# Kernel tuning notes

Measured on AMD Instinct MI355X. Metric: run time of the kernel, lower is better.

Reference implementation:

```python
import jax, jax.numpy as jnp
import numpy as np

LN_EPS = 1e-5

def layer_norm(x, gamma, beta):
    mu = jnp.mean(x, axis=-1, keepdims=True)
    var = jnp.mean(jnp.square(x - mu), axis=-1, keepdims=True)
    return (x - mu) * jax.lax.rsqrt(var + LN_EPS) * gamma + beta

def setup_inputs() -> dict:
    key = jax.random.key(0)
    ks = jax.random.split(key, 10)
    B, C, N = 8, 256, 4096
    s = 1.0 / np.sqrt(C)
    inp = {
        "x": jax.random.normal(ks[0], (B, C, N), dtype=jnp.float32),
        "W_qkv": jax.random.uniform(ks[1], (C, C), jnp.float32, -s, s),            # Linear(dim, dim, bias=False)
        "W_mlp": jax.random.uniform(ks[2], (2 * C, 2 * C), jnp.float32, -0.5 * s, 0.5 * s),
        "b_mlp": jax.random.uniform(ks[3], (2 * C,), jnp.float32, -0.5 * s, 0.5 * s),
        "g1": jnp.ones((4 * C,), jnp.float32),
        "beta1": jnp.zeros((4 * C,), jnp.float32),
        "W_res": jax.random.uniform(ks[4], (C, 4 * C), jnp.float32, -0.25 * s, 0.25 * s),  # Linear(4*dim, dim, bias=False)
        "g2": jnp.ones((C,), jnp.float32),
        "beta2": jnp.zeros((C,), jnp.float32),
    }
    return inp

def reference(x, W_qkv, W_mlp, b_mlp, g1, beta1, W_res, g2, beta2):
    # x: (B, C, N) channels-first -> (B, N, C)
    NITER = 2  # niter_heads
    x = jnp.swapaxes(x, 1, 2)
    x = x @ W_qkv.T                                   # shared_qkv, (B, N, C)
    v = jax.lax.stop_gradient(x)                      # x.clone().detach()
    for _ in range(NITER):
        # first_context = x^T @ v : (B, C, C)
        ctx = jnp.einsum('bnc,bnd->bcd', x, v)
        out = jax.nn.softmax(x, axis=-1) @ ctx        # (B, N, C)
        cat1 = jnp.concatenate([out, v], axis=-1)     # (B, N, 2C)
        mlp = jax.nn.relu(cat1 @ W_mlp.T + b_mlp)     # (B, N, 2C)
        cat2 = jnp.concatenate([cat1, mlp], axis=-1)  # (B, N, 4C)
        # dropout layers are identity in eval mode
        v = layer_norm(cat2, g1, beta1) @ W_res.T + x # residual_mlp + skip
        v = layer_norm(x + v, g2, beta2)
    return jnp.swapaxes(v, 1, 2)                      # back to (B, C, N)
```

## Files before the change

kernel.cpp:

```cpp
#include <hip/hip_runtime.h>
#include <cstdint>
#include <cstddef>


using u16 = unsigned short;
using short8 = __attribute__((ext_vector_type(8))) short;
using bf16x8 = __attribute__((ext_vector_type(8))) __bf16;
using f32x4  = __attribute__((ext_vector_type(4))) float;
using i32x4  = __attribute__((ext_vector_type(4))) int;
using u16x4  = __attribute__((ext_vector_type(4))) u16;
using u16x8  = __attribute__((ext_vector_type(8))) u16;

__device__ __forceinline__ float b2f(u16 u) {
    union { unsigned u32; float f; } c; c.u32 = ((unsigned)u) << 16; return c.f;
}
__device__ __forceinline__ u16 f2b(float f) {
    union { float f; unsigned u; } c; c.f = f;
    unsigned r = c.u + 0x7FFFu + ((c.u >> 16) & 1u);
    return (u16)(r >> 16);
}
__device__ __forceinline__ void cvt(u16 a,  u16& o)   { o = a; }
__device__ __forceinline__ void cvt(float a, u16& o)  { o = f2b(a); }
__device__ __forceinline__ void cvt(float a, float& o){ o = a; }
__device__ __forceinline__ void cvt(u16 a,  float& o) { o = b2f(a); }

__device__ __forceinline__ void glds16(const u16* g, short* l) {
    __builtin_amdgcn_global_load_lds(
        (const __attribute__((address_space(1))) void*)g,
        (__attribute__((address_space(3))) void*)l, 16, 0, 0);
}

template<int MODE, int TRF>
__global__ __launch_bounds__(512)
void gemm_bt(const u16* __restrict__ A, const u16* __restrict__ A2,
             const u16* __restrict__ A3,
             int lda, int lda2, int lda3, int kSplit,
             const u16* __restrict__ B, int ldb, long strA, long strB,
             int statStride, int kChunk, int nKsplit,
             float* __restrict__ outF, u16* __restrict__ outB,
             long sOF, long sOB, int ldo,
             const u16* __restrict__ Xres,
             const float* __restrict__ bias,
             const float2* __restrict__ stats,
             const float* __restrict__ g, const float* __restrict__ be)
{
    __shared__ short lsA[128 * 64];
    __shared__ short lsB[128 * 64];

    const unsigned gx = gridDim.x, gy = gridDim.y;
    const unsigned nwg = gx * gy * gridDim.z;
    unsigned lin = blockIdx.x + gx * (blockIdx.y + gy * blockIdx.z);
    lin = (lin & 7u) * (nwg >> 3) + (lin >> 3);
    const unsigned sbx = lin % gx;
    const unsigned rest = lin / gx;
    const unsigned sby = rest % gy;
    const unsigned sbz = rest / gy;

    const int bz    = (int)sbz;
    const int batch = bz / nKsplit;
    const int ks    = bz - batch * nKsplit;
    const u16* Ab = A + (size_t)batch * strA;
    const u16* Bb = B + (size_t)batch * strB;
    const int colBase = (int)sbx * 128;
    const int rowBase = (int)sby * 128;
    const int k0 = ks * kChunk;
    const int k1 = k0 + kChunk;

    const int t    = threadIdx.x;
    const int sRow = t >> 3;
    const int sKl  = (t & 7) << 3;
    const int sKg  = (((t & 7) ^ (sRow & 7)) << 3);

    const int lane = t & 63;
    const int w    = t >> 6;
    const int wr   = (w >> 1) * 32;
    const int wc   = (w & 1) * 64;
    const int mrow = lane & 15;
    const int q    = lane >> 4;

    short* ldA0 = &lsA[w * 512];
    short* ldA1 = &lsA[4096 + w * 512];
    short* ldB0 = &lsB[w * 512];
    short* ldB1 = &lsB[4096 + w * 512];

    float2 st0 = {0.f, 0.f}, st1 = {0.f, 0.f};
    if (TRF == 1) {
        const int sb = batch * statStride + rowBase;
        const float2 t0 = stats[sb + sRow];
        const float2 t1 = stats[sb + sRow + 64];
        st0 = make_float2(0.f, 1.f / t0.y);
        st1 = make_float2(0.f, 1.f / t1.y);
    }

    auto aPtr = [&](int rloc, int kn) -> const u16* {
        const int arow = rowBase + rloc + sRow;
        if (TRF == 2) {
            if (kn < 256)      return A  + (size_t)arow * lda  + kn + sKg;
            else if (kn < 512) return A2 + (size_t)arow * lda2 + (kn - 256) + sKg;
            else               return A3 + (size_t)arow * lda3 + (kn - 512) + sKg;
        } else if (TRF == 3) {
            if (kn < kSplit)   return Ab + (size_t)arow * lda + kn + sKg;
            return A2 + (size_t)arow * lda2 + (kn - kSplit) + sKg;
        }
        return Ab + (size_t)arow * lda + kn + sKg;
    };
    auto loadX = [&](int rloc, int kn, float2 st) -> i32x4 {
        const int arow = rowBase + rloc + sRow;
        i32x4 raw = *(const i32x4*)(Ab + (size_t)arow * lda + kn + sKg);
        short8 h = __builtin_bit_cast(short8, raw);
        short8 o;
#pragma unroll
        for (int i = 0; i < 8; i++) {
            float v = b2f((u16)h[i]);
            v = __expf(v - st.x) * st.y;
            o[i] = (short)f2b(v);
        }
        return __builtin_bit_cast(i32x4, o);
    };

    const f32x4 fzero = {0.f, 0.f, 0.f, 0.f};
    f32x4 acc[2][4];
#pragma unroll
    for (int i = 0; i < 2; i++)
#pragma unroll
        for (int j = 0; j < 4; j++) acc[i][j] = fzero;

    const u16* pB0 = Bb + (size_t)(colBase + sRow) * ldb + sKg;
    const u16* pB1 = pB0 + (size_t)64 * ldb;
    const u16* pA0 = nullptr; const u16* pA1 = nullptr;
    if (TRF == 0) {
        pA0 = Ab + (size_t)(rowBase + sRow) * lda + sKg;
        pA1 = pA0 + (size_t)64 * lda;
    }

    const int rsw = mrow & 7;
    const int kc0 = (((0 * 4 + q) ^ rsw) << 3);
    const int kc1 = (((1 * 4 + q) ^ rsw) << 3);

    i32x4 a0, a1;
    if (TRF == 1) {
        a0 = loadX(0,  k0, st0);
        a1 = loadX(64, k0, st1);
    }

    for (int kk = k0; kk < k1; kk += 64) {
        if (TRF == 1) {
            *(i32x4*)&lsA[sRow * 64 + sKl]        = a0;
            *(i32x4*)&lsA[(sRow + 64) * 64 + sKl] = a1;
        } else if (TRF == 0) {
            glds16(pA0 + kk, ldA0);
            glds16(pA1 + kk, ldA1);
        } else {
            glds16(aPtr(0,  kk), ldA0);
            glds16(aPtr(64, kk), ldA1);
        }
        glds16(pB0 + kk, ldB0);
        glds16(pB1 + kk, ldB1);
        __syncthreads();
        const int kn = kk + 64;
        if (TRF == 1 && kn < k1) {
            a0 = loadX(0,  kn, st0);
            a1 = loadX(64, kn, st1);
        }
#pragma unroll
        for (int h = 0; h < 2; h++) {
            const int kc = h ? kc1 : kc0;
            bf16x8 af[2], bfr[4];
#pragma unroll
            for (int mi = 0; mi < 2; mi++)
                af[mi] = __builtin_bit_cast(bf16x8,
                    *(const short8*)&lsA[(wr + mi * 16 + mrow) * 64 + kc]);
#pragma unroll
            for (int ni = 0; ni < 4; ni++)
                bfr[ni] = __builtin_bit_cast(bf16x8,
                    *(const short8*)&lsB[(wc + ni * 16 + mrow) * 64 + kc]);
#pragma unroll
            for (int mi = 0; mi < 2; mi++)
#pragma unroll
                for (int ni = 0; ni < 4; ni++)
                    acc[mi][ni] = __builtin_amdgcn_mfma_f32_16x16x32_bf16(
                        af[mi], bfr[ni], acc[mi][ni], 0, 0, 0);
        }
        __syncthreads();
    }

    if (MODE == 5) {
        u16* XT = const_cast<u16*>(Xres);
        float2* sm = const_cast<float2*>(stats);
        float rsum[2][4] = {{0.f,0.f,0.f,0.f},{0.f,0.f,0.f,0.f}};
#pragma unroll
        for (int mi = 0; mi < 2; mi++) {
#pragma unroll
            for (int ni = 0; ni < 4; ni++) {
                const int col  = colBase + wc + ni * 16 + mrow;
                const int row0 = rowBase + wr + mi * 16 + q * 4;
                u16x4 hv;
#pragma unroll
                for (int r = 0; r < 4; r++) {
                    const u16 h = f2b(acc[mi][ni][r]);
                    hv[r] = h;
                    outB[(size_t)(row0 + r) * ldo + col] = h;
                    rsum[mi][r] += __expf(b2f(h));
                }
                *(u16x4*)(XT + (size_t)(row0 >> 12) * 1048576
                             + (size_t)col * 4096 + (row0 & 4095)) = hv;
            }
        }
#pragma unroll
        for (int mi = 0; mi < 2; mi++)
#pragma unroll
            for (int r = 0; r < 4; r++) {
                float s = rsum[mi][r];
                s += __shfl_xor(s, 1); s += __shfl_xor(s, 2);
                s += __shfl_xor(s, 4); s += __shfl_xor(s, 8);
                if (mrow == 0)
                    atomicAdd(&sm[rowBase + wr + mi * 16 + q * 4 + r].y, s);
            }
        return;
    }

#pragma unroll
    for (int mi = 0; mi < 2; mi++) {
#pragma unroll
        for (int ni = 0; ni < 4; ni++) {
            const int col = colBase + wc + ni * 16 + mrow;
#pragma unroll
            for (int r = 0; r < 4; r++) {
                const int row = rowBase + wr + mi * 16 + q * 4 + r;
                float v = acc[mi][ni][r];
                if (MODE == 0) {
                    outB[(size_t)batch * sOB + (size_t)row * ldo + col] = f2b(v);
                } else if (MODE == 1) {
                    outB[((size_t)batch * nKsplit + ks) * sOB
                         + (size_t)row * ldo + col] = f2b(v);
                } else if (MODE == 3) {
                    v += bias[col];
                    v = v > 0.f ? v : 0.f;
                    outB[(size_t)row * ldo + col] = f2b(v);
                } else if (MODE == 4) {
                    const float2 ln = stats[row];
                    v = ln.y * (v - ln.x * g[col]) + be[col]
                        + 2.f * b2f(Xres[(size_t)row * 256 + col]);
                    outB[(size_t)row * ldo + col] = f2b(v);
                }
            }
        }
    }
}

template<typename TIN, typename TOUT>
__global__ __launch_bounds__(256)
void transpose_k(const TIN* __restrict__ in, TOUT* __restrict__ out,
                 int R, int Cc, long sIn, long sOut)
{
    __shared__ TOUT tile[32][33];
    const int b = blockIdx.z;
    const TIN* ib = in + (size_t)b * sIn;
    TOUT* ob = out + (size_t)b * sOut;
    const int c0 = blockIdx.x * 32, r0 = blockIdx.y * 32;
    const int tx = threadIdx.x & 31, ty = threadIdx.x >> 5;
#pragma unroll
    for (int i = 0; i < 32; i += 8)
        cvt(ib[(size_t)(r0 + ty + i) * Cc + c0 + tx], tile[ty + i][tx]);
    __syncthreads();
#pragma unroll
    for (int i = 0; i < 32; i += 8)
        ob[(size_t)(c0 + ty + i) * R + r0 + tx] = tile[tx][ty + i];
}

__global__ __launch_bounds__(256)
void stats1024_k(const u16* __restrict__ OUT, const u16* __restrict__ V,
                 const u16* __restrict__ MLPo, float2* __restrict__ st)
{
    const int wave = threadIdx.x >> 6, lane = threadIdx.x & 63;
    const size_t row = (size_t)blockIdx.x * 4 + wave;
    const int c = lane * 16;
    const u16* src;
    if (c < 256)       src = OUT  + row * 256 + c;
    else if (c < 512)  src = V    + row * 256 + (c - 256);
    else               src = MLPo + row * 512 + (c - 512);
    short8 r0 = *(const short8*)(src);
    short8 r1 = *(const short8*)(src + 8);
    float s = 0.f, s2 = 0.f;
#pragma unroll
    for (int i = 0; i < 8; i++) {
        const float a = b2f((u16)r0[i]), b = b2f((u16)r1[i]);
        s += a + b; s2 += a * a + b * b;
    }
    for (int o = 32; o > 0; o >>= 1) { s += __shfl_xor(s, o); s2 += __shfl_xor(s2, o); }
    const float mean = s * (1.f / 1024.f);
    const float var  = s2 * (1.f / 1024.f) - mean * mean;
    if (lane == 0) st[row] = make_float2(mean, rsqrtf(var + 1e-5f));
}

template<typename OUTT, bool WRITE_VB>
__global__ __launch_bounds__(256)
void ln256t_k(const u16* __restrict__ Tb, const float* __restrict__ g,
              const float* __restrict__ be, u16* __restrict__ Vb,
              OUTT* __restrict__ outT)
{
    constexpr int STRIDE = (sizeof(OUTT) == 2) ? 266 : 261;
    __shared__ OUTT tile[32 * STRIDE];
    const int wid = threadIdx.x >> 6, lane = threadIdx.x & 63;
    const int bx = blockIdx.x;
    const size_t r0 = (size_t)bx * 32;
    const int b  = bx >> 7;
    const int n0 = (bx & 127) * 32;

#pragma unroll
    for (int j = 0; j < 8; j++) {
        const int lr = wid * 8 + j;
        const size_t row = r0 + lr;
        const u16x4 tb = *(const u16x4*)(Tb + row * 256 + lane * 4);
        const float x0 = b2f(tb.x), x1 = b2f(tb.y), x2 = b2f(tb.z), x3 = b2f(tb.w);
        float s  = x0 + x1 + x2 + x3;
        float s2 = x0 * x0 + x1 * x1 + x2 * x2 + x3 * x3;
        for (int o = 32; o > 0; o >>= 1) { s += __shfl_xor(s, o); s2 += __shfl_xor(s2, o); }
        const float mean = s * (1.f / 256.f);
        const float var  = s2 * (1.f / 256.f) - mean * mean;
        const float rstd = rsqrtf(var + 1e-5f);
        const int c = lane * 4;
        float4 ov = { (x0 - mean) * rstd * g[c + 0] + be[c + 0],
                      (x1 - mean) * rstd * g[c + 1] + be[c + 1],
                      (x2 - mean) * rstd * g[c + 2] + be[c + 2],
                      (x3 - mean) * rstd * g[c + 3] + be[c + 3] };
        if (WRITE_VB) {
            u16x4 vb = { f2b(ov.x), f2b(ov.y), f2b(ov.z), f2b(ov.w) };
            *(u16x4*)(Vb + row * 256 + c) = vb;
        }
        OUTT* tl = &tile[lr * STRIDE + c];
        cvt(ov.x, tl[0]); cvt(ov.y, tl[1]); cvt(ov.z, tl[2]); cvt(ov.w, tl[3]);
    }
    __syncthreads();

    const int c = threadIdx.x;
    OUTT* dst = outT + ((size_t)b * 256 + c) * 4096 + n0;
    if (sizeof(OUTT) == 2) {
#pragma unroll
        for (int k = 0; k < 4; k++) {
            u16x8 v;
#pragma unroll
            for (int i = 0; i < 8; i++) v[i] = *(const u16*)&tile[(k * 8 + i) * STRIDE + c];
            *(u16x8*)((u16*)dst + k * 8) = v;
        }
    } else {
#pragma unroll
        for (int k = 0; k < 8; k++) {
            float4 v;
            v.x = *(const float*)&tile[(k * 4 + 0) * STRIDE + c];
            v.y = *(const float*)&tile[(k * 4 + 1) * STRIDE + c];
            v.z = *(const float*)&tile[(k * 4 + 2) * STRIDE + c];
            v.w = *(const float*)&tile[(k * 4 + 3) * STRIDE + c];
            *(float4*)((float*)dst + k * 4) = v;
        }
    }
}

__global__ __launch_bounds__(256)
void ctxreduce_k(const u16* __restrict__ ctxp, u16* __restrict__ ctxb)
{
    const int i = blockIdx.x * 256 + threadIdx.x;
    const int batch  = i >> 14;
    const int within = i & 16383;
    const u16x4* src = (const u16x4*)ctxp + (size_t)batch * 16 * 16384 + within;
    float4 s = {0.f, 0.f, 0.f, 0.f};
#pragma unroll
    for (int ks = 0; ks < 16; ks++) {
        const u16x4 v = src[(size_t)ks * 16384];
        s.x += b2f(v.x); s.y += b2f(v.y); s.z += b2f(v.z); s.w += b2f(v.w);
    }
    u16x4 o = { f2b(s.x), f2b(s.y), f2b(s.z), f2b(s.w) };
    ((u16x4*)ctxb)[i] = o;
}

__global__ __launch_bounds__(256)
void wconv_k(const float* __restrict__ Wq, const float* __restrict__ Wm,
             u16* __restrict__ oq, u16* __restrict__ om)
{
    const int i = blockIdx.x * 256 + threadIdx.x;
    const float* src; u16* dst; int j;
    if (i < 16384) { src = Wq; dst = oq; j = i; }
    else           { src = Wm; dst = om; j = i - 16384; }
    const float4 v = ((const float4*)src)[j];
    u16x4 o = { f2b(v.x), f2b(v.y), f2b(v.z), f2b(v.w) };
    ((u16x4*)dst)[j] = o;
}

__global__ __launch_bounds__(256)
void wresprep_k(const float* __restrict__ Wres, const float* __restrict__ g1,
                const float* __restrict__ be1, u16* __restrict__ Wr_b,
                float* __restrict__ sg, float* __restrict__ br,
                float2* __restrict__ smst)
{
    const int tid = blockIdx.x * 256 + threadIdx.x;
    smst[tid * 2]     = make_float2(0.f, 0.f);
    smst[tid * 2 + 1] = make_float2(0.f, 0.f);

    const int wv = threadIdx.x >> 6, lane = threadIdx.x & 63;
    const int row = blockIdx.x * 4 + wv;
    const float* src = Wres + (size_t)row * 1024;
    float s = 0.f, b = 0.f;
#pragma unroll
    for (int j = 0; j < 4; j++) {
        const int c = j * 256 + lane * 4;
        const float4 w  = *(const float4*)(src + c);
        const float4 gg = *(const float4*)(g1 + c);
        const float4 bb = *(const float4*)(be1 + c);
        const float4 wg = { w.x * gg.x, w.y * gg.y, w.z * gg.z, w.w * gg.w };
        u16x4 o = { f2b(wg.x), f2b(wg.y), f2b(wg.z), f2b(wg.w) };
        *(u16x4*)(Wr_b + (size_t)row * 1024 + c) = o;
        s += wg.x + wg.y + wg.z + wg.w;
        b += w.x * bb.x + w.y * bb.y + w.z * bb.z + w.w * bb.w;
    }
    for (int o = 32; o > 0; o >>= 1) { s += __shfl_xor(s, o); b += __shfl_xor(b, o); }
    if (lane == 0) { sg[row] = s; br[row] = b; }
}

extern "C" void kernel_launch(void* const* d_in, const int* in_sizes, int n_in,
                              void* d_out, int out_size, void* d_ws, size_t ws_size,
                              hipStream_t stream)
{
    (void)in_sizes; (void)n_in; (void)out_size; (void)ws_size;
    const float* x    = (const float*)d_in[0];
    const float* Wqkv = (const float*)d_in[1];
    const float* Wmlp = (const float*)d_in[2];
    const float* bmlp = (const float*)d_in[3];
    const float* g1   = (const float*)d_in[4];
    const float* be1  = (const float*)d_in[5];
    const float* Wres = (const float*)d_in[6];
    const float* g2   = (const float*)d_in[7];
    const float* be2  = (const float*)d_in[8];

    char* ws = (char*)d_ws;
    u16*    Xb   = (u16*)ws;    ws += (size_t)16777216;
    u16*    XT   = (u16*)ws;    ws += (size_t)16777216;
    u16*    Vb   = (u16*)ws;    ws += (size_t)16777216;
    u16*    VT2  = (u16*)ws;    ws += (size_t)16777216;
    u16*    OUT  = (u16*)ws;    ws += (size_t)16777216;
    u16*    MLPo = (u16*)ws;    ws += (size_t)33554432;
    u16*    Tb   = (u16*)ws;    ws += (size_t)16777216;
    u16*    ctxp = (u16*)ws;    ws += (size_t)16777216;
    u16*    ctxb = (u16*)ws;    ws += (size_t)1048576;
    float2* smst = (float2*)ws; ws += (size_t)262144;
    float2* lnst = (float2*)ws; ws += (size_t)262144;
    u16*    Wq_b = (u16*)ws;    ws += (size_t)131072;
    u16*    Wm_b = (u16*)ws;    ws += (size_t)524288;
    u16*    Wr_b = (u16*)ws;    ws += (size_t)524288;
    float*  sg   = (float*)ws;  ws += (size_t)1024;
    float*  br   = (float*)ws;  ws += (size_t)1024;
    u16*    xt   = MLPo;

    wconv_k<<<dim3(320), 256, 0, stream>>>(Wqkv, Wmlp, Wq_b, Wm_b);
    wresprep_k<<<dim3(64), 256, 0, stream>>>(Wres, g1, be1, Wr_b, sg, br, smst);

    transpose_k<float, u16><<<dim3(128, 8, 8), 256, 0, stream>>>(
        x, xt, 256, 4096, 256L * 4096, 4096L * 256);

    gemm_bt<5, 0><<<dim3(2, 256, 1), 512, 0, stream>>>(
        xt, nullptr, nullptr, 256, 0, 0, 0, Wq_b, 256, 0, 0, 0, 256, 1,
        nullptr, Xb, 0, 0, 256, XT, nullptr, smst, nullptr, nullptr);

    const u16* VTcur = XT;
    const u16* Vcur  = Xb;

    for (int it = 0; it < 2; ++it) {
        gemm_bt<1, 0><<<dim3(2, 2, 128), 512, 0, stream>>>(
            VTcur, nullptr, nullptr, 4096, 0, 0, 0, XT, 4096,
            1048576, 1048576, 0, 256, 16,
            nullptr, ctxp, 0, 65536, 256, nullptr, nullptr, nullptr, nullptr, nullptr);
        ctxreduce_k<<<dim3(512), 256, 0, stream>>>(ctxp, ctxb);

        gemm_bt<0, 1><<<dim3(2, 32, 8), 512, 0, stream>>>(
            Xb, nullptr, nullptr, 256, 0, 0, 0, ctxb, 256,
            1048576, 65536, 4096, 256, 1,
            nullptr, OUT, 0, 1048576, 256, nullptr, nullptr, smst, nullptr, nullptr);

        gemm_bt<3, 3><<<dim3(4, 256, 1), 512, 0, stream>>>(
            OUT, Vcur, nullptr, 256, 256, 0, 256, Wm_b, 512, 0, 0, 0, 512, 1,
            nullptr, MLPo, 0, 0, 512, nullptr, bmlp, nullptr, nullptr, nullptr);

        stats1024_k<<<dim3(8192), 256, 0, stream>>>(OUT, Vcur, MLPo, lnst);

        gemm_bt<4, 2><<<dim3(2, 256, 1), 512, 0, stream>>>(
            OUT, Vcur, MLPo, 256, 256, 512, 0, Wr_b, 1024, 0, 0, 0, 1024, 1,
            nullptr, Tb, 0, 0, 256, Xb, nullptr, lnst, sg, br);

        if (it == 0) {
            ln256t_k<u16, true><<<dim3(1024), 256, 0, stream>>>(
                Tb, g2, be2, Vb, VT2);
            VTcur = VT2;
            Vcur  = Vb;
        } else {
            ln256t_k<float, false><<<dim3(1024), 256, 0, stream>>>(
                Tb, g2, be2, nullptr, (float*)d_out);
        }
    }
}
```

Measured before the change: 327.9 us.

## Fuse LayerNorm-1024 row statistics into the residual GEMM's A-tile loads

Removes the separate stats1024 kernel, which re-read OUT, V and MLPo to compute per-row mean and variance. The residual GEMM (MODE 4) now accumulates sum and sum-of-squares from each A tile already staged in shared memory, reduces them across lanes and through a small LDS array, then applies the normalization in the epilogue. This saves one kernel launch and a full 1024-wide activation read per iteration. The cost is extra LDS reads and ALU work inside the GEMM main loop, plus an added barrier in the epilogue.

```diff
diff --git a/kernel.cpp b/kernel.cpp
--- a/kernel.cpp
+++ b/kernel.cpp
@@ -46,6 +46,7 @@
 {
     __shared__ short lsA[128 * 64];
     __shared__ short lsB[128 * 64];
+    __shared__ float2 lstat[128];
 
     const unsigned gx = gridDim.x, gy = gridDim.y;
     const unsigned nwg = gx * gy * gridDim.z;
@@ -136,6 +137,8 @@
     const int rsw = mrow & 7;
     const int kc0 = (((0 * 4 + q) ^ rsw) << 3);
     const int kc1 = (((1 * 4 + q) ^ rsw) << 3);
+
+    float stA = 0.f, stA2 = 0.f, stB = 0.f, stB2 = 0.f;
 
     i32x4 a0, a1;
     if (TRF == 1) {
@@ -162,6 +165,17 @@
             a0 = loadX(0,  kn, st0);
             a1 = loadX(64, kn, st1);
         }
+        if (MODE == 4) {
+            short8 c0 = *(const short8*)&lsA[sRow * 64 + sKl];
+            short8 c1 = *(const short8*)&lsA[(sRow + 64) * 64 + sKl];
+#pragma unroll
+            for (int i = 0; i < 8; i++) {
+                const float v0 = b2f((u16)c0[i]);
+                const float v1 = b2f((u16)c1[i]);
+                stA += v0; stA2 += v0 * v0;
+                stB += v1; stB2 += v1 * v1;
+            }
+        }
 #pragma unroll
         for (int h = 0; h < 2; h++) {
             const int kc = h ? kc1 : kc0;
@@ -216,6 +230,45 @@
                 if (mrow == 0)
                     atomicAdd(&sm[rowBase + wr + mi * 16 + q * 4 + r].y, s);
             }
+        return;
+    }
+
+    if (MODE == 4) {
+        for (int o = 1; o <= 4; o <<= 1) {
+            stA  += __shfl_xor(stA,  o);  stA2 += __shfl_xor(stA2, o);
+            stB  += __shfl_xor(stB,  o);  stB2 += __shfl_xor(stB2, o);
+        }
+        if ((lane & 7) == 0) {
+            lstat[sRow]      = make_float2(stA, stA2);
+            lstat[sRow + 64] = make_float2(stB, stB2);
+        }
+        __syncthreads();
+        float mean_[2][4], rstd_[2][4];
+#pragma unroll
+        for (int mi = 0; mi < 2; mi++)
+#pragma unroll
+            for (int r = 0; r < 4; r++) {
+                const float2 s = lstat[wr + mi * 16 + q * 4 + r];
+                const float mean = s.x * (1.f / 1024.f);
+                const float var  = s.y * (1.f / 1024.f) - mean * mean;
+                mean_[mi][r] = mean;
+                rstd_[mi][r] = rsqrtf(var + 1e-5f);
+            }
+#pragma unroll
+        for (int mi = 0; mi < 2; mi++) {
+#pragma unroll
+            for (int ni = 0; ni < 4; ni++) {
+                const int col = colBase + wc + ni * 16 + mrow;
+#pragma unroll
+                for (int r = 0; r < 4; r++) {
+                    const int row = rowBase + wr + mi * 16 + q * 4 + r;
+                    float v = acc[mi][ni][r];
+                    v = rstd_[mi][r] * (v - mean_[mi][r] * g[col]) + be[col]
+                        + 2.f * b2f(Xres[(size_t)row * 256 + col]);
+                    outB[(size_t)row * ldo + col] = f2b(v);
+                }
+            }
+        }
         return;
     }
 
@@ -237,11 +290,6 @@
                     v += bias[col];
                     v = v > 0.f ? v : 0.f;
                     outB[(size_t)row * ldo + col] = f2b(v);
-                } else if (MODE == 4) {
-                    const float2 ln = stats[row];
-                    v = ln.y * (v - ln.x * g[col]) + be[col]
-                        + 2.f * b2f(Xres[(size_t)row * 256 + col]);
-                    outB[(size_t)row * ldo + col] = f2b(v);
                 }
             }
         }
@@ -266,31 +314,6 @@
 #pragma unroll
     for (int i = 0; i < 32; i += 8)
         ob[(size_t)(c0 + ty + i) * R + r0 + tx] = tile[tx][ty + i];
-}
-
-__global__ __launch_bounds__(256)
-void stats1024_k(const u16* __restrict__ OUT, const u16* __restrict__ V,
-                 const u16* __restrict__ MLPo, float2* __restrict__ st)
-{
-    const int wave = threadIdx.x >> 6, lane = threadIdx.x & 63;
-    const size_t row = (size_t)blockIdx.x * 4 + wave;
-    const int c = lane * 16;
-    const u16* src;
-    if (c < 256)       src = OUT  + row * 256 + c;
-    else if (c < 512)  src = V    + row * 256 + (c - 256);
-    else               src = MLPo + row * 512 + (c - 512);
-    short8 r0 = *(const short8*)(src);
-    short8 r1 = *(const short8*)(src + 8);
-    float s = 0.f, s2 = 0.f;
-#pragma unroll
-    for (int i = 0; i < 8; i++) {
-        const float a = b2f((u16)r0[i]), b = b2f((u16)r1[i]);
-        s += a + b; s2 += a * a + b * b;
-    }
-    for (int o = 32; o > 0; o >>= 1) { s += __shfl_xor(s, o); s2 += __shfl_xor(s2, o); }
-    const float mean = s * (1.f / 1024.f);
-    const float var  = s2 * (1.f / 1024.f) - mean * mean;
-    if (lane == 0) st[row] = make_float2(mean, rsqrtf(var + 1e-5f));
 }
 
 template<typename OUTT, bool WRITE_VB>
@@ -442,7 +465,6 @@
     u16*    ctxp = (u16*)ws;    ws += (size_t)16777216;
     u16*    ctxb = (u16*)ws;    ws += (size_t)1048576;
     float2* smst = (float2*)ws; ws += (size_t)262144;
-    float2* lnst = (float2*)ws; ws += (size_t)262144;
     u16*    Wq_b = (u16*)ws;    ws += (size_t)131072;
     u16*    Wm_b = (u16*)ws;    ws += (size_t)524288;
     u16*    Wr_b = (u16*)ws;    ws += (size_t)524288;
@@ -479,11 +501,9 @@
             OUT, Vcur, nullptr, 256, 256, 0, 256, Wm_b, 512, 0, 0, 0, 512, 1,
             nullptr, MLPo, 0, 0, 512, nullptr, bmlp, nullptr, nullptr, nullptr);
 
-        stats1024_k<<<dim3(8192), 256, 0, stream>>>(OUT, Vcur, MLPo, lnst);
-
         gemm_bt<4, 2><<<dim3(2, 256, 1), 512, 0, stream>>>(
             OUT, Vcur, MLPo, 256, 256, 512, 0, Wr_b, 1024, 0, 0, 0, 1024, 1,
-            nullptr, Tb, 0, 0, 256, Xb, nullptr, lnst, sg, br);
+            nullptr, Tb, 0, 0, 256, Xb, nullptr, nullptr, sg, br);
 
         if (it == 0) {
             ln256t_k<u16, true><<<dim3(1024), 256, 0, stream>>>(
```

Result: no change. 326.4 us (-0.5%).
